# Kernel tuning notes

Measured on AMD Instinct MI355X. Metric: run time of the kernel, lower is better.

The kernel has to match this reference:

```python
import jax, jax.numpy as jnp
import numpy as np

B, S, D, H = 2, 2048, 1024, 16
DK = D // H


def setup_inputs() -> dict:
    key = jax.random.key(0)
    ks = jax.random.split(key, 12)
    sc = 0.02
    inp = {
        'query': jax.random.normal(ks[0], (B, S, D), jnp.float32),
        'key': jax.random.normal(ks[1], (B, S, D), jnp.float32),
        'value': jax.random.normal(ks[2], (B, S, D), jnp.float32),
        # causal mask: positions with mask==0 are disallowed (matches masked_fill(mask==0, -inf))
        'mask': jnp.broadcast_to(jnp.tril(jnp.ones((S, S), jnp.int32)), (B, S, S)),
        'Wq': jax.random.normal(ks[3], (D, D), jnp.float32) * sc,
        'bq': jax.random.normal(ks[4], (D,), jnp.float32) * sc,
        'Wk': jax.random.normal(ks[5], (D, D), jnp.float32) * sc,
        'bk': jax.random.normal(ks[6], (D,), jnp.float32) * sc,
        'Wv': jax.random.normal(ks[7], (D, D), jnp.float32) * sc,
        'bv': jax.random.normal(ks[8], (D,), jnp.float32) * sc,
        'Wo': jax.random.normal(ks[9], (D, D), jnp.float32) * sc,
        'bo': jax.random.normal(ks[10], (D,), jnp.float32) * sc,
    }
    return inp


def reference(query, key, value, mask, Wq, bq, Wk, bk, Wv, bv, Wo, bo):
    # Linear projections (torch Linear: x @ W.T + b), split heads -> [B,H,S,DK]
    def proj(x, W, b):
        return (x @ W.T + b).reshape(B, S, H, DK).transpose(0, 2, 1, 3)

    q = proj(query, Wq, bq)
    k = proj(key, Wk, bk)
    v = proj(value, Wv, bv)

    scores = jnp.einsum('bhqd,bhkd->bhqk', q, k) / jnp.sqrt(jnp.float32(DK))
    # mask unsqueezed over head dim: [B,1,S,S]
    scores = jnp.where(mask[:, None, :, :] == 0, -jnp.inf, scores)
    p = jax.nn.softmax(scores, axis=-1)
    x = jnp.einsum('bhqk,bhkd->bhqd', p, v)  # [B,H,S,DK]
    x = x.transpose(0, 2, 1, 3).reshape(B, S, D)
    return x @ Wo.T + bo
```

## Files before the change

kernel.cpp:

```cpp
#include <hip/hip_runtime.h>
#include <hip/hip_bf16.h>
#include <math.h>

#define BATCH 2
#define SEQ 2048
#define DMODEL 1024
#define NHEAD 16
#define DHEAD 64
#define MTOT (BATCH*SEQ)

typedef __attribute__((ext_vector_type(8))) short bf16x8;
typedef __attribute__((ext_vector_type(4))) short short4v;
typedef __attribute__((ext_vector_type(4))) float f32x4;

static __device__ inline short f2bs(float x) {
    __hip_bfloat16 b = __float2bfloat16(x);
    return *reinterpret_cast<short*>(&b);
}

struct ConvArgs {
    const float* src[7];
    unsigned short* dst[7];
    int nblk[7];
};

__global__ __launch_bounds__(256)
void convert_bf16_kernel(ConvArgs a)
{
    int b = blockIdx.x;
    int r = 0;
    while (b >= a.nblk[r]) { b -= a.nblk[r]; ++r; }
    const float* s = a.src[r];
    unsigned short* d = a.dst[r];
    const int base = b * 2048 + threadIdx.x * 8;
    const float4 f0 = *reinterpret_cast<const float4*>(&s[base]);
    const float4 f1 = *reinterpret_cast<const float4*>(&s[base + 4]);
    bf16x8 o;
    o[0] = f2bs(f0.x); o[1] = f2bs(f0.y); o[2] = f2bs(f0.z); o[3] = f2bs(f0.w);
    o[4] = f2bs(f1.x); o[5] = f2bs(f1.y); o[6] = f2bs(f1.z); o[7] = f2bs(f1.w);
    *reinterpret_cast<bf16x8*>(&d[base]) = o;
}

template<int SPLIT>
static __device__ __forceinline__
void gemm_core(const short* __restrict__ Xg, const short* __restrict__ Wg,
               const float* __restrict__ bias, void* __restrict__ outp,
               float scale, int m0, int n0)
{
    __shared__ short Xs[2][128 * 64];
    __shared__ short Wt[2][128 * 64];

    const int t    = threadIdx.x;
    const int lane = t & 63;
    const int w    = t >> 6;
    const int wm   = w >> 1, wn = w & 1;
    const int m_   = lane & 15, g = lane >> 4;

    const int sr  = t >> 1;
    const int sc0 = (t & 1) * 4;

    f32x4 acc[4][4] = {};
    bf16x8 xr[4], wr[4];

    #pragma unroll
    for (int c = 0; c < 4; ++c) {
        xr[c] = *reinterpret_cast<const bf16x8*>(&Xg[(size_t)(m0 + sr) * DMODEL + (sc0 + c) * 8]);
        wr[c] = *reinterpret_cast<const bf16x8*>(&Wg[(size_t)(n0 + sr) * DMODEL + (sc0 + c) * 8]);
    }
    #pragma unroll
    for (int c = 0; c < 4; ++c) {
        const int byo = sr * 128 + (((sc0 + c) * 16) ^ ((sr & 7) << 4));
        *reinterpret_cast<bf16x8*>((char*)Xs[0] + byo) = xr[c];
        *reinterpret_cast<bf16x8*>((char*)Wt[0] + byo) = wr[c];
    }
    __syncthreads();

    for (int kt = 0; kt < DMODEL / 64; ++kt) {
        const int cur = kt & 1;
        const bool more = (kt < DMODEL / 64 - 1);

        if (more) {
            const int k0 = (kt + 1) * 64;
            #pragma unroll
            for (int c = 0; c < 4; ++c) {
                xr[c] = *reinterpret_cast<const bf16x8*>(&Xg[(size_t)(m0 + sr) * DMODEL + k0 + (sc0 + c) * 8]);
                wr[c] = *reinterpret_cast<const bf16x8*>(&Wg[(size_t)(n0 + sr) * DMODEL + k0 + (sc0 + c) * 8]);
            }
        }

        bf16x8 af[4][2], bfr[4][2];
        #pragma unroll
        for (int mt = 0; mt < 4; ++mt) {
            const int row = wm * 64 + mt * 16 + m_;
            #pragma unroll
            for (int kc = 0; kc < 2; ++kc)
                af[mt][kc] = *reinterpret_cast<const bf16x8*>(
                    (char*)Xs[cur] + row * 128 + ((kc * 64 + g * 16) ^ ((row & 7) << 4)));
        }
        #pragma unroll
        for (int nt = 0; nt < 4; ++nt) {
            const int row = wn * 64 + nt * 16 + m_;
            #pragma unroll
            for (int kc = 0; kc < 2; ++kc)
                bfr[nt][kc] = *reinterpret_cast<const bf16x8*>(
                    (char*)Wt[cur] + row * 128 + ((kc * 64 + g * 16) ^ ((row & 7) << 4)));
        }

        __builtin_amdgcn_s_setprio(1);
        #pragma unroll
        for (int mt = 0; mt < 4; ++mt)
            #pragma unroll
            for (int nt = 0; nt < 4; ++nt)
                #pragma unroll
                for (int kc = 0; kc < 2; ++kc)
                    acc[mt][nt] = __builtin_amdgcn_mfma_f32_16x16x32_bf16(
                        af[mt][kc], bfr[nt][kc], acc[mt][nt], 0, 0, 0);
        __builtin_amdgcn_s_setprio(0);

        if (more) {
            #pragma unroll
            for (int c = 0; c < 4; ++c) {
                const int byo = sr * 128 + (((sc0 + c) * 16) ^ ((sr & 7) << 4));
                *reinterpret_cast<bf16x8*>((char*)Xs[cur ^ 1] + byo) = xr[c];
                *reinterpret_cast<bf16x8*>((char*)Wt[cur ^ 1] + byo) = wr[c];
            }
        }
        __syncthreads();
    }

    float bv[4];
    #pragma unroll
    for (int nt = 0; nt < 4; ++nt) bv[nt] = bias[n0 + wn * 64 + nt * 16 + m_];

    #pragma unroll
    for (int mt = 0; mt < 4; ++mt) {
        #pragma unroll
        for (int r = 0; r < 4; ++r) {
            const int row = m0 + wm * 64 + mt * 16 + g * 4 + r;
            const int b = row >> 11;
            const int s = row & 2047;
            #pragma unroll
            for (int nt = 0; nt < 4; ++nt) {
                const int n = n0 + wn * 64 + nt * 16 + m_;
                const float c = (acc[mt][nt][r] + bv[nt]) * scale;
                if (SPLIT) {
                    const int h = n >> 6, dk = n & 63;
                    ((__hip_bfloat16*)outp)[(((size_t)(b * NHEAD + h)) * SEQ + s) * DHEAD + dk]
                        = __float2bfloat16(c);
                } else {
                    ((float*)outp)[(size_t)row * DMODEL + n] = c;
                }
            }
        }
    }
}

struct TrioArgs {
    const short* X[3];
    const short* W[3];
    const float* bias[3];
    __hip_bfloat16* out[3];
    float scale[3];
};

__global__ __launch_bounds__(256)
void gemm_qkv_kernel(TrioArgs a)
{
    const int which = blockIdx.x >> 8;
    const int tile  = blockIdx.x & 255;
    const int n0 = (tile & 7) * 128;
    const int m0 = (tile >> 3) * 128;
    gemm_core<1>(a.X[which], a.W[which], a.bias[which], a.out[which],
                 a.scale[which], m0, n0);
}

__global__ __launch_bounds__(256)
void gemm_out_kernel(const short* __restrict__ X, const short* __restrict__ W,
                     const float* __restrict__ bias, float* __restrict__ out)
{
    gemm_core<0>(X, W, bias, out, 1.0f, blockIdx.y * 128, blockIdx.x * 128);
}

__global__ __launch_bounds__(512, 4)
void attn_mfma_kernel(const __hip_bfloat16* __restrict__ Q,
                      const __hip_bfloat16* __restrict__ K,
                      const __hip_bfloat16* __restrict__ V,
                      __hip_bfloat16* __restrict__ ctx)
{
    __shared__ short Ks[64 * 64];
    __shared__ short Vts[64 * 64];
    __shared__ short Ps[8 * 16 * 72];

    const int t    = threadIdx.x;
    const int lane = t & 63;
    const int w    = t >> 6;
    const int wq   = w & 3;
    const int side = w >> 2;
    const int m    = lane & 15;
    const int g    = lane >> 4;

    const int bid = blockIdx.x;
    const int swz = (bid & 7) * 64 + (bid >> 3);
    const int bh  = swz >> 4;
    const int pr  = swz & 15;
    const int qtA = pr, qtB = 31 - pr;
    const int myqt = side ? qtB : qtA;
    const int q0   = myqt * 64;

    const __hip_bfloat16* Qb = Q + (size_t)bh * SEQ * DHEAD;
    const __hip_bfloat16* Kb = K + (size_t)bh * SEQ * DHEAD;
    const __hip_bfloat16* Vb = V + (size_t)bh * SEQ * DHEAD;

    bf16x8 qf[2];
    #pragma unroll
    for (int c = 0; c < 2; ++c)
        qf[c] = *reinterpret_cast<const bf16x8*>(
            &Qb[(size_t)(q0 + 16 * wq + m) * DHEAD + c * 32 + 8 * g]);

    f32x4 o[4] = {};
    float mr = -INFINITY, lr = 0.0f;

    short* Pw = Ps + w * 16 * 72;

    for (int kt = 0; kt <= qtB; ++kt) {
        const int k0 = kt * 64;

        {
            const int krow = t >> 3;
            const int kch  = t & 7;
            const bf16x8 kv = *reinterpret_cast<const bf16x8*>(
                &Kb[(size_t)(k0 + krow) * DHEAD + kch * 8]);
            *reinterpret_cast<bf16x8*>((char*)Ks +
                (((krow * 128) + kch * 16) ^ ((krow & 7) << 4))) = kv;

            const int vk = t & 63;
            const int d0 = (t >> 6) * 8;
            const bf16x8 vv = *reinterpret_cast<const bf16x8*>(
                &Vb[(size_t)(k0 + vk) * DHEAD + d0]);
            #pragma unroll
            for (int j = 0; j < 8; ++j) {
                const int d = d0 + j;
                *reinterpret_cast<short*>((char*)Vts +
                    (((d * 128) + vk * 2) ^ ((d & 7) << 4))) = vv[j];
            }
        }
        __syncthreads();

        if (kt <= myqt) {
            f32x4 s[4] = {};
            __builtin_amdgcn_s_setprio(1);
            #pragma unroll
            for (int ct = 0; ct < 4; ++ct) {
                const int krow = ct * 16 + m;
                #pragma unroll
                for (int c = 0; c < 2; ++c) {
                    const bf16x8 kf = *reinterpret_cast<const bf16x8*>((char*)Ks +
                        (((krow * 128) + c * 64 + 16 * g) ^ ((krow & 7) << 4)));
                    s[ct] = __builtin_amdgcn_mfma_f32_16x16x32_bf16(kf, qf[c], s[ct], 0, 0, 0);
                }
            }
            __builtin_amdgcn_s_setprio(0);

            if (kt == myqt) {
                const int qr = 16 * wq + m;
                #pragma unroll
                for (int ct = 0; ct < 4; ++ct)
                    #pragma unroll
                    for (int r = 0; r < 4; ++r)
                        if (ct * 16 + 4 * g + r > qr) s[ct][r] = -INFINITY;
            }

            float pmax = -INFINITY;
            #pragma unroll
            for (int ct = 0; ct < 4; ++ct) {
                const float a = fmaxf(fmaxf(s[ct][0], s[ct][1]),
                                      fmaxf(s[ct][2], s[ct][3]));
                pmax = fmaxf(pmax, a);
            }
            pmax = fmaxf(pmax, __shfl_xor(pmax, 16, 64));
            pmax = fmaxf(pmax, __shfl_xor(pmax, 32, 64));

            const float mnew = fmaxf(mr, pmax);
            const float scl  = __expf(mr - mnew);
            mr = mnew;

            float psum = 0.0f;
            #pragma unroll
            for (int ct = 0; ct < 4; ++ct) {
                #pragma unroll
                for (int r = 0; r < 4; ++r) {
                    s[ct][r] = __expf(s[ct][r] - mnew);
                    psum += s[ct][r];
                }
            }
            psum += __shfl_xor(psum, 16, 64);
            psum += __shfl_xor(psum, 32, 64);
            lr = lr * scl + psum;

            #pragma unroll
            for (int dt = 0; dt < 4; ++dt)
                #pragma unroll
                for (int r = 0; r < 4; ++r)
                    o[dt][r] *= scl;

            #pragma unroll
            for (int ct = 0; ct < 4; ++ct) {
                short4v p4;
                p4[0] = f2bs(s[ct][0]); p4[1] = f2bs(s[ct][1]);
                p4[2] = f2bs(s[ct][2]); p4[3] = f2bs(s[ct][3]);
                *reinterpret_cast<short4v*>(&Pw[m * 72 + ct * 16 + 4 * g]) = p4;
            }

            bf16x8 pf[2];
            #pragma unroll
            for (int c = 0; c < 2; ++c)
                pf[c] = *reinterpret_cast<const bf16x8*>(&Pw[m * 72 + c * 32 + 8 * g]);

            __builtin_amdgcn_s_setprio(1);
            #pragma unroll
            for (int dt = 0; dt < 4; ++dt) {
                const int vrow = dt * 16 + m;
                #pragma unroll
                for (int c = 0; c < 2; ++c) {
                    const bf16x8 vf = *reinterpret_cast<const bf16x8*>((char*)Vts +
                        (((vrow * 128) + c * 64 + 16 * g) ^ ((vrow & 7) << 4)));
                    o[dt] = __builtin_amdgcn_mfma_f32_16x16x32_bf16(vf, pf[c], o[dt], 0, 0, 0);
                }
            }
            __builtin_amdgcn_s_setprio(0);
        }
        __syncthreads();
    }

    const int b = bh >> 4;
    const int h = bh & 15;
    const float inv = 1.0f / lr;
    const int row = q0 + 16 * wq + m;
    short* dst = (short*)&ctx[((size_t)(b * SEQ) + row) * DMODEL + h * DHEAD];
    #pragma unroll
    for (int dt = 0; dt < 4; ++dt) {
        short4v p4;
        p4[0] = f2bs(o[dt][0] * inv); p4[1] = f2bs(o[dt][1] * inv);
        p4[2] = f2bs(o[dt][2] * inv); p4[3] = f2bs(o[dt][3] * inv);
        *reinterpret_cast<short4v*>(dst + dt * 16 + 4 * g) = p4;
    }
}

extern "C" void kernel_launch(void* const* d_in, const int* in_sizes, int n_in,
                              void* d_out, int out_size, void* d_ws, size_t ws_size,
                              hipStream_t stream)
{
    const float* query = (const float*)d_in[0];
    const float* key   = (const float*)d_in[1];
    const float* value = (const float*)d_in[2];
    const float* Wq = (const float*)d_in[4];
    const float* bq = (const float*)d_in[5];
    const float* Wk = (const float*)d_in[6];
    const float* bk = (const float*)d_in[7];
    const float* Wv = (const float*)d_in[8];
    const float* bv = (const float*)d_in[9];
    const float* Wo = (const float*)d_in[10];
    const float* bo = (const float*)d_in[11];
    float* out = (float*)d_out;

    char* ws = (char*)d_ws;
    const size_t MB = 1024 * 1024;
    unsigned short* xq  = (unsigned short*)(ws + 0 * MB);
    unsigned short* xk  = (unsigned short*)(ws + 8 * MB);
    unsigned short* xv  = (unsigned short*)(ws + 16 * MB);
    unsigned short* wqb = (unsigned short*)(ws + 24 * MB);
    unsigned short* wkb = (unsigned short*)(ws + 26 * MB);
    unsigned short* wvb = (unsigned short*)(ws + 28 * MB);
    unsigned short* wob = (unsigned short*)(ws + 30 * MB);
    __hip_bfloat16* qb  = (__hip_bfloat16*)(ws + 32 * MB);
    __hip_bfloat16* kb  = (__hip_bfloat16*)(ws + 40 * MB);
    __hip_bfloat16* vb  = (__hip_bfloat16*)(ws + 48 * MB);
    __hip_bfloat16* ctx = (__hip_bfloat16*)(ws + 56 * MB);

    ConvArgs ca;
    ca.src[0] = query; ca.dst[0] = xq;  ca.nblk[0] = 2048;
    ca.src[1] = key;   ca.dst[1] = xk;  ca.nblk[1] = 2048;
    ca.src[2] = value; ca.dst[2] = xv;  ca.nblk[2] = 2048;
    ca.src[3] = Wq;    ca.dst[3] = wqb; ca.nblk[3] = 512;
    ca.src[4] = Wk;    ca.dst[4] = wkb; ca.nblk[4] = 512;
    ca.src[5] = Wv;    ca.dst[5] = wvb; ca.nblk[5] = 512;
    ca.src[6] = Wo;    ca.dst[6] = wob; ca.nblk[6] = 512;
    convert_bf16_kernel<<<dim3(8192), dim3(256), 0, stream>>>(ca);

    TrioArgs ta;
    ta.X[0] = (const short*)xq; ta.W[0] = (const short*)wqb; ta.bias[0] = bq;
    ta.out[0] = qb; ta.scale[0] = 0.125f;
    ta.X[1] = (const short*)xk; ta.W[1] = (const short*)wkb; ta.bias[1] = bk;
    ta.out[1] = kb; ta.scale[1] = 1.0f;
    ta.X[2] = (const short*)xv; ta.W[2] = (const short*)wvb; ta.bias[2] = bv;
    ta.out[2] = vb; ta.scale[2] = 1.0f;
    gemm_qkv_kernel<<<dim3(768), dim3(256), 0, stream>>>(ta);

    attn_mfma_kernel<<<dim3(512), dim3(512), 0, stream>>>(qb, kb, vb, ctx);

    gemm_out_kernel<<<dim3(8, 32), dim3(256), 0, stream>>>(
        (const short*)ctx, (const short*)wob, bo, out);
}
```

Baseline: 133.5 us.

## Use direct global-to-LDS loads and double-buffer K/V tiles in attention

The GEMM staging now uses global_load_lds, which writes 16-byte chunks straight into shared memory with an XOR-swizzled source column, instead of loading into registers and storing to LDS. The attention kernel gains double-buffered K and V tiles. K is prefetched with direct LDS loads, and V is loaded into registers early and transposed into the other buffer after the compute, so one barrier per iteration is removed. This is meant to overlap global loads with MFMA work and lower register pressure. It doubles the attention LDS footprint, which may reduce occupancy, and it relies on the async LDS writes being complete by the barrier.

```diff
diff --git a/kernel.cpp b/kernel.cpp
--- a/kernel.cpp
+++ b/kernel.cpp
@@ -16,6 +16,13 @@
 static __device__ inline short f2bs(float x) {
     __hip_bfloat16 b = __float2bfloat16(x);
     return *reinterpret_cast<short*>(&b);
+}
+
+static __device__ __forceinline__ void gload16(const void* g, void* l) {
+    __builtin_amdgcn_global_load_lds(
+        (const __attribute__((address_space(1))) unsigned int*)g,
+        (__attribute__((address_space(3))) unsigned int*)l,
+        16, 0, 0);
 }
 
 struct ConvArgs {
@@ -56,37 +63,29 @@
     const int wm   = w >> 1, wn = w & 1;
     const int m_   = lane & 15, g = lane >> 4;
 
-    const int sr  = t >> 1;
-    const int sc0 = (t & 1) * 4;
+    const int rl = lane >> 3;
+    const int cs = (lane & 7) ^ rl;
+
+    auto stage = [&](int k0, int buf) {
+        #pragma unroll
+        for (int c = 0; c < 4; ++c) {
+            const int rowb = 32 * w + 8 * c;
+            gload16(Xg + (size_t)(m0 + rowb + rl) * DMODEL + k0 + cs * 8,
+                    &Xs[buf][rowb * 64]);
+            gload16(Wg + (size_t)(n0 + rowb + rl) * DMODEL + k0 + cs * 8,
+                    &Wt[buf][rowb * 64]);
+        }
+    };
 
     f32x4 acc[4][4] = {};
-    bf16x8 xr[4], wr[4];
-
-    #pragma unroll
-    for (int c = 0; c < 4; ++c) {
-        xr[c] = *reinterpret_cast<const bf16x8*>(&Xg[(size_t)(m0 + sr) * DMODEL + (sc0 + c) * 8]);
-        wr[c] = *reinterpret_cast<const bf16x8*>(&Wg[(size_t)(n0 + sr) * DMODEL + (sc0 + c) * 8]);
-    }
-    #pragma unroll
-    for (int c = 0; c < 4; ++c) {
-        const int byo = sr * 128 + (((sc0 + c) * 16) ^ ((sr & 7) << 4));
-        *reinterpret_cast<bf16x8*>((char*)Xs[0] + byo) = xr[c];
-        *reinterpret_cast<bf16x8*>((char*)Wt[0] + byo) = wr[c];
-    }
+
+    stage(0, 0);
     __syncthreads();
 
+    int cur = 0;
     for (int kt = 0; kt < DMODEL / 64; ++kt) {
-        const int cur = kt & 1;
         const bool more = (kt < DMODEL / 64 - 1);
-
-        if (more) {
-            const int k0 = (kt + 1) * 64;
-            #pragma unroll
-            for (int c = 0; c < 4; ++c) {
-                xr[c] = *reinterpret_cast<const bf16x8*>(&Xg[(size_t)(m0 + sr) * DMODEL + k0 + (sc0 + c) * 8]);
-                wr[c] = *reinterpret_cast<const bf16x8*>(&Wg[(size_t)(n0 + sr) * DMODEL + k0 + (sc0 + c) * 8]);
-            }
-        }
+        if (more) stage((kt + 1) * 64, cur ^ 1);
 
         bf16x8 af[4][2], bfr[4][2];
         #pragma unroll
@@ -117,15 +116,8 @@
                         af[mt][kc], bfr[nt][kc], acc[mt][nt], 0, 0, 0);
         __builtin_amdgcn_s_setprio(0);
 
-        if (more) {
-            #pragma unroll
-            for (int c = 0; c < 4; ++c) {
-                const int byo = sr * 128 + (((sc0 + c) * 16) ^ ((sr & 7) << 4));
-                *reinterpret_cast<bf16x8*>((char*)Xs[cur ^ 1] + byo) = xr[c];
-                *reinterpret_cast<bf16x8*>((char*)Wt[cur ^ 1] + byo) = wr[c];
-            }
-        }
         __syncthreads();
+        cur ^= 1;
     }
 
     float bv[4];
@@ -187,8 +179,8 @@
                       const __hip_bfloat16* __restrict__ V,
                       __hip_bfloat16* __restrict__ ctx)
 {
-    __shared__ short Ks[64 * 64];
-    __shared__ short Vts[64 * 64];
+    __shared__ short Ks[2][64 * 64];
+    __shared__ short Vts[2][64 * 64];
     __shared__ short Ps[8 * 16 * 72];
 
     const int t    = threadIdx.x;
@@ -211,6 +203,28 @@
     const __hip_bfloat16* Kb = K + (size_t)bh * SEQ * DHEAD;
     const __hip_bfloat16* Vb = V + (size_t)bh * SEQ * DHEAD;
 
+    const int krl = lane >> 3;
+    const int kcs = (lane & 7) ^ krl;
+    const int vk  = t & 63;
+    const int vd0 = (t >> 6) * 8;
+
+    bf16x8 vreg;
+    auto stageK = [&](int k0s, int buf) {
+        gload16(Kb + (size_t)(k0s + 8 * w + krl) * DHEAD + kcs * 8,
+                &Ks[buf][w * 512]);
+    };
+    auto loadV = [&](int k0s) {
+        vreg = *reinterpret_cast<const bf16x8*>(&Vb[(size_t)(k0s + vk) * DHEAD + vd0]);
+    };
+    auto writeV = [&](int buf) {
+        #pragma unroll
+        for (int j = 0; j < 8; ++j) {
+            const int d = vd0 + j;
+            *reinterpret_cast<short*>((char*)Vts[buf] +
+                (((d * 128) + vk * 2) ^ ((d & 7) << 4))) = vreg[j];
+        }
+    };
+
     bf16x8 qf[2];
     #pragma unroll
     for (int c = 0; c < 2; ++c)
@@ -222,29 +236,18 @@
 
     short* Pw = Ps + w * 16 * 72;
 
+    stageK(0, 0);
+    loadV(0);
+    writeV(0);
+    __syncthreads();
+
+    int cur = 0;
     for (int kt = 0; kt <= qtB; ++kt) {
-        const int k0 = kt * 64;
-
-        {
-            const int krow = t >> 3;
-            const int kch  = t & 7;
-            const bf16x8 kv = *reinterpret_cast<const bf16x8*>(
-                &Kb[(size_t)(k0 + krow) * DHEAD + kch * 8]);
-            *reinterpret_cast<bf16x8*>((char*)Ks +
-                (((krow * 128) + kch * 16) ^ ((krow & 7) << 4))) = kv;
-
-            const int vk = t & 63;
-            const int d0 = (t >> 6) * 8;
-            const bf16x8 vv = *reinterpret_cast<const bf16x8*>(
-                &Vb[(size_t)(k0 + vk) * DHEAD + d0]);
-            #pragma unroll
-            for (int j = 0; j < 8; ++j) {
-                const int d = d0 + j;
-                *reinterpret_cast<short*>((char*)Vts +
-                    (((d * 128) + vk * 2) ^ ((d & 7) << 4))) = vv[j];
-            }
-        }
-        __syncthreads();
+        const bool more = (kt < qtB);
+        if (more) {
+            stageK((kt + 1) * 64, cur ^ 1);
+            loadV((kt + 1) * 64);
+        }
 
         if (kt <= myqt) {
             f32x4 s[4] = {};
@@ -254,7 +257,7 @@
                 const int krow = ct * 16 + m;
                 #pragma unroll
                 for (int c = 0; c < 2; ++c) {
-                    const bf16x8 kf = *reinterpret_cast<const bf16x8*>((char*)Ks +
+                    const bf16x8 kf = *reinterpret_cast<const bf16x8*>((char*)Ks[cur] +
                         (((krow * 128) + c * 64 + 16 * g) ^ ((krow & 7) << 4)));
                     s[ct] = __builtin_amdgcn_mfma_f32_16x16x32_bf16(kf, qf[c], s[ct], 0, 0, 0);
                 }
@@ -322,14 +325,17 @@
                 const int vrow = dt * 16 + m;
                 #pragma unroll
                 for (int c = 0; c < 2; ++c) {
-                    const bf16x8 vf = *reinterpret_cast<const bf16x8*>((char*)Vts +
+                    const bf16x8 vf = *reinterpret_cast<const bf16x8*>((char*)Vts[cur] +
                         (((vrow * 128) + c * 64 + 16 * g) ^ ((vrow & 7) << 4)));
                     o[dt] = __builtin_amdgcn_mfma_f32_16x16x32_bf16(vf, pf[c], o[dt], 0, 0, 0);
                 }
             }
             __builtin_amdgcn_s_setprio(0);
         }
+
+        if (more) writeV(cur ^ 1);
         __syncthreads();
+        cur ^= 1;
     }
 
     const int b = bh >> 4;
```

Result: slower. 137.0 us (+2.6%).

## Double-buffer K/V tiles with async global-to-LDS K loads in attention

Applied to the files above, without the earlier changes.

Attention K and V tiles are now double-buffered in LDS. The next tile is prefetched while the current one is computed: K goes through global_load_lds direct-to-LDS loads and V is loaded into registers early and written transposed after compute. This removes one barrier per iteration and hides global load latency behind the MFMA work. In exchange LDS use doubles, which may lower occupancy, and only half the threads do the staging, each with more work.

```diff
diff --git a/kernel.cpp b/kernel.cpp
--- a/kernel.cpp
+++ b/kernel.cpp
@@ -16,6 +16,13 @@
 static __device__ inline short f2bs(float x) {
     __hip_bfloat16 b = __float2bfloat16(x);
     return *reinterpret_cast<short*>(&b);
+}
+
+static __device__ __forceinline__ void gload16(const void* g, void* l) {
+    __builtin_amdgcn_global_load_lds(
+        (const __attribute__((address_space(1))) unsigned int*)g,
+        (__attribute__((address_space(3))) unsigned int*)l,
+        16, 0, 0);
 }
 
 struct ConvArgs {
@@ -187,8 +194,8 @@
                       const __hip_bfloat16* __restrict__ V,
                       __hip_bfloat16* __restrict__ ctx)
 {
-    __shared__ short Ks[64 * 64];
-    __shared__ short Vts[64 * 64];
+    __shared__ short Ks[2][64 * 64];
+    __shared__ short Vts[2][64 * 64];
     __shared__ short Ps[8 * 16 * 72];
 
     const int t    = threadIdx.x;
@@ -211,6 +218,40 @@
     const __hip_bfloat16* Kb = K + (size_t)bh * SEQ * DHEAD;
     const __hip_bfloat16* Vb = V + (size_t)bh * SEQ * DHEAD;
 
+    const int sKrb = 16 * (w & 3);
+    const int krl  = lane >> 3;
+    const int kcs  = (lane & 7) ^ krl;
+    const int vk   = t & 63;
+    const int vd0  = ((t >> 6) & 3) * 16;
+
+    bf16x8 vreg0, vreg1;
+    auto stageK = [&](int k0s, int buf) {
+        #pragma unroll
+        for (int c2 = 0; c2 < 2; ++c2) {
+            const int rb = sKrb + 8 * c2;
+            gload16(Kb + (size_t)(k0s + rb + krl) * DHEAD + kcs * 8,
+                    &Ks[buf][rb * 64]);
+        }
+    };
+    auto loadV = [&](int k0s) {
+        vreg0 = *reinterpret_cast<const bf16x8*>(&Vb[(size_t)(k0s + vk) * DHEAD + vd0]);
+        vreg1 = *reinterpret_cast<const bf16x8*>(&Vb[(size_t)(k0s + vk) * DHEAD + vd0 + 8]);
+    };
+    auto writeV = [&](int buf) {
+        #pragma unroll
+        for (int j = 0; j < 8; ++j) {
+            const int d = vd0 + j;
+            *reinterpret_cast<short*>((char*)Vts[buf] +
+                (((d * 128) + vk * 2) ^ ((d & 7) << 4))) = vreg0[j];
+        }
+        #pragma unroll
+        for (int j = 0; j < 8; ++j) {
+            const int d = vd0 + 8 + j;
+            *reinterpret_cast<short*>((char*)Vts[buf] +
+                (((d * 128) + vk * 2) ^ ((d & 7) << 4))) = vreg1[j];
+        }
+    };
+
     bf16x8 qf[2];
     #pragma unroll
     for (int c = 0; c < 2; ++c)
@@ -222,29 +263,16 @@
 
     short* Pw = Ps + w * 16 * 72;
 
+    if (t < 256) { stageK(0, 0); loadV(0); writeV(0); }
+    __syncthreads();
+
+    int cur = 0;
     for (int kt = 0; kt <= qtB; ++kt) {
-        const int k0 = kt * 64;
-
-        {
-            const int krow = t >> 3;
-            const int kch  = t & 7;
-            const bf16x8 kv = *reinterpret_cast<const bf16x8*>(
-                &Kb[(size_t)(k0 + krow) * DHEAD + kch * 8]);
-            *reinterpret_cast<bf16x8*>((char*)Ks +
-                (((krow * 128) + kch * 16) ^ ((krow & 7) << 4))) = kv;
-
-            const int vk = t & 63;
-            const int d0 = (t >> 6) * 8;
-            const bf16x8 vv = *reinterpret_cast<const bf16x8*>(
-                &Vb[(size_t)(k0 + vk) * DHEAD + d0]);
-            #pragma unroll
-            for (int j = 0; j < 8; ++j) {
-                const int d = d0 + j;
-                *reinterpret_cast<short*>((char*)Vts +
-                    (((d * 128) + vk * 2) ^ ((d & 7) << 4))) = vv[j];
-            }
-        }
-        __syncthreads();
+        const bool more = (kt < qtB);
+        if (t < 256 && more) {
+            stageK((kt + 1) * 64, cur ^ 1);
+            loadV((kt + 1) * 64);
+        }
 
         if (kt <= myqt) {
             f32x4 s[4] = {};
@@ -254,7 +282,7 @@
                 const int krow = ct * 16 + m;
                 #pragma unroll
                 for (int c = 0; c < 2; ++c) {
-                    const bf16x8 kf = *reinterpret_cast<const bf16x8*>((char*)Ks +
+                    const bf16x8 kf = *reinterpret_cast<const bf16x8*>((char*)Ks[cur] +
                         (((krow * 128) + c * 64 + 16 * g) ^ ((krow & 7) << 4)));
                     s[ct] = __builtin_amdgcn_mfma_f32_16x16x32_bf16(kf, qf[c], s[ct], 0, 0, 0);
                 }
@@ -322,14 +350,17 @@
                 const int vrow = dt * 16 + m;
                 #pragma unroll
                 for (int c = 0; c < 2; ++c) {
-                    const bf16x8 vf = *reinterpret_cast<const bf16x8*>((char*)Vts +
+                    const bf16x8 vf = *reinterpret_cast<const bf16x8*>((char*)Vts[cur] +
                         (((vrow * 128) + c * 64 + 16 * g) ^ ((vrow & 7) << 4)));
                     o[dt] = __builtin_amdgcn_mfma_f32_16x16x32_bf16(vf, pf[c], o[dt], 0, 0, 0);
                 }
             }
             __builtin_amdgcn_s_setprio(0);
         }
+
+        if (t < 256 && more) writeV(cur ^ 1);
         __syncthreads();
+        cur ^= 1;
     }
 
     const int b = bh >> 4;
```

After: 123.1 us. 1.08x faster.
